# Kernel tuning notes

Hardware: AMD Instinct MI355X
Metric: run time of the kernel (lower is better)

## Reference

```python
import jax, jax.numpy as jnp
import numpy as np

N_NODES = 8192
N_EDGES = 65536


def _segment_softmax(scores, seg_ids, num_segments):
    # scores: [E, 1], seg_ids: [E] -> softmax over edges sharing the same dst
    m = jax.ops.segment_max(scores, seg_ids, num_segments=num_segments)  # [N,1]
    e = jnp.exp(scores - m[seg_ids])
    denom = jax.ops.segment_sum(e, seg_ids, num_segments=num_segments)   # [N,1]
    return e / denom[seg_ids]


def setup_inputs() -> dict:
    key = jax.random.key(0)
    ks = jax.random.split(key, 12)
    s = lambda fin: 1.0 / np.sqrt(fin)
    inp = {
        'n_f': jax.random.normal(ks[0], (N_NODES, 1024), jnp.float32),
        'word2vec': jax.random.normal(ks[1], (N_NODES, 300), jnp.float32),
        's_f': jax.random.normal(ks[2], (N_EDGES, 16), jnp.float32),
        'src': jax.random.randint(ks[3], (N_EDGES,), 0, N_NODES),
        'dst': jax.random.randint(ks[4], (N_EDGES,), 0, N_NODES),
        'We': jax.random.normal(ks[5], (2064, 1024), jnp.float32) * s(2064),
        'be': jnp.zeros((1024,), jnp.float32),
        'Wel': jax.random.normal(ks[6], (600, 600), jnp.float32) * s(600),
        'bel': jnp.zeros((600,), jnp.float32),
        'Wa': jax.random.normal(ks[7], (1024, 1), jnp.float32) * s(1024),
        'ba': jnp.zeros((1,), jnp.float32),
        'Wal': jax.random.normal(ks[8], (600, 1), jnp.float32) * s(600),
        'bal': jnp.zeros((1,), jnp.float32),
        'Wn': jax.random.normal(ks[9], (2048, 1024), jnp.float32) * s(2048),
        'bn': jnp.zeros((1024,), jnp.float32),
        'Wnl': jax.random.normal(ks[10], (600, 300), jnp.float32) * s(600),
        'bnl': jnp.zeros((300,), jnp.float32),
    }
    return inp


def reference(n_f, word2vec, s_f, src, dst,
              We, be, Wel, bel, Wa, ba, Wal, bal, Wn, bn, Wnl, bnl):
    # ---- edge apply (H_H_EdgeApplyModule) ----
    src_nf = n_f[src]                                    # [E,1024] gather
    feat = jnp.concatenate([src_nf, s_f, n_f[dst]], axis=1)  # [E,2064]
    e_f = jax.nn.relu(feat @ We + be)                    # [E,1024]
    feat_lang = jnp.concatenate([word2vec[src], word2vec[dst]], axis=1)  # [E,600]
    e_f_lang = jax.nn.relu(feat_lang @ Wel + bel)        # [E,600]

    # ---- edge attention (E_AttentionModule1): scalar score per edge ----
    a_feat = e_f @ Wa + ba                               # [E,1]
    a_feat_lang = e_f_lang @ Wal + bal                   # [E,1]

    # ---- reduce: mailbox softmax over incoming edges per dst node ----
    alpha = _segment_softmax(a_feat, dst, N_NODES)       # [E,1]
    alpha_lang = _segment_softmax(a_feat_lang, dst, N_NODES)
    z_f = jax.ops.segment_sum(alpha * (src_nf + e_f), dst, num_segments=N_NODES)      # [N,1024]
    z_f_lang = jax.ops.segment_sum(alpha_lang * word2vec[src], dst, num_segments=N_NODES)  # [N,300]

    # ---- node apply (H_NodeApplyModule) ----
    new_n_f = jax.nn.relu(jnp.concatenate([n_f, z_f], axis=1) @ Wn + bn)              # [N,1024]
    new_n_f_lang = jax.nn.relu(jnp.concatenate([word2vec, z_f_lang], axis=1) @ Wnl + bnl)  # [N,300]
    return new_n_f, new_n_f_lang
```

## Files before the change

### kernel.cpp

```cpp
#include <hip/hip_runtime.h>
#include <hip/hip_bf16.h>

#define N_NODES 8192
#define N_EDGES 65536
#define OUT0_ELEMS ((size_t)N_NODES * 1024)

using bf16 = __hip_bfloat16;
typedef __attribute__((ext_vector_type(8))) short short8;
typedef __attribute__((ext_vector_type(4))) float f32x4;

__device__ __forceinline__ float b2f(bf16 x) { return __bfloat162float(x); }
__device__ __forceinline__ bf16 f2b(float x) { return __float2bfloat16(x); }
__device__ __forceinline__ unsigned short bbits(float x)
{
  union { bf16 h; unsigned short u; } v; v.h = f2b(x); return v.u;
}
__device__ __forceinline__ unsigned pack2(float a, float b)
{
  return (unsigned)bbits(a) | ((unsigned)bbits(b) << 16);
}
__device__ __forceinline__ float4 ld4b(const bf16* p)
{
  uint2 u = *(const uint2*)p;
  float4 r;
  r.x = __uint_as_float(u.x << 16);
  r.y = __uint_as_float(u.x & 0xffff0000u);
  r.z = __uint_as_float(u.y << 16);
  r.w = __uint_as_float(u.y & 0xffff0000u);
  return r;
}
__device__ __forceinline__ void st4b(bf16* p, float a, float b, float c, float d)
{
  uint2 v; v.x = pack2(a, b); v.y = pack2(c, d);
  *(uint2*)p = v;
}

__global__ void GNN_27650999451833_kernel() {}

__global__ void gnn6_zero(int* __restrict__ p, int n)
{
  int i = blockIdx.x * blockDim.x + threadIdx.x;
  if (i < n) p[i] = 0;
}

__global__ __launch_bounds__(256)
void gnn7_cvt(const float* __restrict__ src, bf16* __restrict__ dst, int n8)
{
  int i = blockIdx.x * blockDim.x + threadIdx.x;
  if (i < n8) {
    float4 a = ((const float4*)src)[2 * i];
    float4 b = ((const float4*)src)[2 * i + 1];
    uint4 p;
    p.x = pack2(a.x, a.y); p.y = pack2(a.z, a.w);
    p.z = pack2(b.x, b.y); p.w = pack2(b.z, b.w);
    ((uint4*)dst)[i] = p;
  }
}

__global__ __launch_bounds__(256)
void gnn8_pad_w2v(const float* __restrict__ src, bf16* __restrict__ dst)
{
  int idx = blockIdx.x * blockDim.x + threadIdx.x;
  if (idx >= N_NODES * 80) return;
  int r = idx / 80, c0 = (idx % 80) * 4;
  float v[4];
#pragma unroll
  for (int j = 0; j < 4; ++j) {
    int c = c0 + j;
    v[j] = (c < 300) ? src[(size_t)r * 300 + c] : 0.f;
  }
  uint2 p; p.x = pack2(v[0], v[1]); p.y = pack2(v[2], v[3]);
  *(uint2*)(dst + (size_t)r * 320 + c0) = p;
}

__global__ __launch_bounds__(256)
void gnn8_pad_Wel(const float* __restrict__ src, bf16* __restrict__ dst)
{
  int idx = blockIdx.x * blockDim.x + threadIdx.x;
  if (idx >= 320 * 320) return;
  int k = idx / 320, c0 = (idx % 320) * 4;
  float v[4];
#pragma unroll
  for (int j = 0; j < 4; ++j) {
    int c = c0 + j;
    float x = 0.f;
    if (k < 300) {
      if (c < 600)       x = src[(size_t)k * 600 + c];
      else if (c < 1200) x = src[(size_t)(300 + k) * 600 + (c - 600)];
    }
    v[j] = x;
  }
  uint2 p; p.x = pack2(v[0], v[1]); p.y = pack2(v[2], v[3]);
  *(uint2*)(dst + (size_t)k * 1280 + c0) = p;
}

__global__ __launch_bounds__(256)
void gnn8_pad_Wnl(const float* __restrict__ src, bf16* __restrict__ dst)
{
  int idx = blockIdx.x * blockDim.x + threadIdx.x;
  if (idx >= 640 * 96) return;
  int k = idx / 96, c0 = (idx % 96) * 4;
  int kr = -1;
  if (k < 300) kr = k;
  else if (k >= 320 && k < 620) kr = k - 20;
  float v[4];
#pragma unroll
  for (int j = 0; j < 4; ++j) {
    int c = c0 + j;
    v[j] = (kr >= 0 && c < 300) ? src[(size_t)kr * 300 + c] : 0.f;
  }
  uint2 p; p.x = pack2(v[0], v[1]); p.y = pack2(v[2], v[3]);
  *(uint2*)(dst + (size_t)k * 384 + c0) = p;
}

__global__ __launch_bounds__(256)
void gnn7_mm_P(const bf16* __restrict__ A, const float* __restrict__ We,
               bf16* __restrict__ P)
{
  __shared__ short As[128 * 40];
  __shared__ short Bs[128 * 40];
  const int t = threadIdx.x;
  const int col0 = blockIdx.x * 128, row0 = blockIdx.y * 128;
  const int lane = t & 63, w = t >> 6, m16 = lane & 15, q = lane >> 4;
  const int wr = w >> 1, wc = w & 1;

  f32x4 acc[4][4];
#pragma unroll
  for (int mi = 0; mi < 4; ++mi)
#pragma unroll
    for (int ni = 0; ni < 4; ++ni) acc[mi][ni] = (f32x4){0.f, 0.f, 0.f, 0.f};

  const int ar = t >> 1, ah = (t & 1) * 16;
  const int bk = t & 31, bn0 = (t >> 5) * 16;

  const bf16* aptr = A + (size_t)(row0 + ar) * 1024 + ah;
  const float* bptr = (col0 < 1024)
      ? (We + (size_t)bk * 1024 + col0 + bn0)
      : (We + (size_t)(1040 + bk) * 1024 + (col0 - 1024) + bn0);

  uint4 a0 = *(const uint4*)(aptr);
  uint4 a1 = *(const uint4*)(aptr + 8);
  float4 b0 = *(const float4*)(bptr);
  float4 b1 = *(const float4*)(bptr + 4);
  float4 b2 = *(const float4*)(bptr + 8);
  float4 b3 = *(const float4*)(bptr + 12);

  for (int k0 = 0; k0 < 1024; k0 += 32) {
    if (k0) __syncthreads();
    *(uint4*)&As[ar * 40 + ah] = a0;
    *(uint4*)&As[ar * 40 + ah + 8] = a1;
    {
      short* brow = &Bs[bn0 * 40 + bk];
      brow[0 * 40] = (short)bbits(b0.x);  brow[1 * 40] = (short)bbits(b0.y);
      brow[2 * 40] = (short)bbits(b0.z);  brow[3 * 40] = (short)bbits(b0.w);
      brow[4 * 40] = (short)bbits(b1.x);  brow[5 * 40] = (short)bbits(b1.y);
      brow[6 * 40] = (short)bbits(b1.z);  brow[7 * 40] = (short)bbits(b1.w);
      brow[8 * 40] = (short)bbits(b2.x);  brow[9 * 40] = (short)bbits(b2.y);
      brow[10 * 40] = (short)bbits(b2.z); brow[11 * 40] = (short)bbits(b2.w);
      brow[12 * 40] = (short)bbits(b3.x); brow[13 * 40] = (short)bbits(b3.y);
      brow[14 * 40] = (short)bbits(b3.z); brow[15 * 40] = (short)bbits(b3.w);
    }
    __syncthreads();
    if (k0 + 32 < 1024) {
      a0 = *(const uint4*)(aptr + k0 + 32);
      a1 = *(const uint4*)(aptr + k0 + 40);
      const float* bp = bptr + (size_t)(k0 + 32) * 1024;
      b0 = *(const float4*)(bp);
      b1 = *(const float4*)(bp + 4);
      b2 = *(const float4*)(bp + 8);
      b3 = *(const float4*)(bp + 12);
    }
    short8 af[4];
#pragma unroll
    for (int mi = 0; mi < 4; ++mi)
      af[mi] = *(const short8*)&As[(wr * 64 + mi * 16 + m16) * 40 + 8 * q];
#pragma unroll
    for (int ni = 0; ni < 4; ++ni) {
      short8 bfv = *(const short8*)&Bs[(wc * 64 + ni * 16 + m16) * 40 + 8 * q];
#pragma unroll
      for (int mi = 0; mi < 4; ++mi)
        acc[mi][ni] =
            __builtin_amdgcn_mfma_f32_16x16x32_bf16(af[mi], bfv, acc[mi][ni], 0, 0, 0);
    }
  }
#pragma unroll
  for (int mi = 0; mi < 4; ++mi)
#pragma unroll
    for (int ni = 0; ni < 4; ++ni) {
      int c = col0 + wc * 64 + ni * 16 + m16;
#pragma unroll
      for (int r = 0; r < 4; ++r)
        P[(size_t)(row0 + wr * 64 + mi * 16 + 4 * q + r) * 2048 + c] =
            f2b(acc[mi][ni][r]);
    }
}

__global__ __launch_bounds__(256)
void gnn7_mm_out_n(const bf16* __restrict__ nf_bf, const bf16* __restrict__ zf,
                   const float* __restrict__ Wn, const float* __restrict__ bn,
                   float* __restrict__ out)
{
  __shared__ short As[128 * 40];
  __shared__ short Bs[128 * 40];
  const int t = threadIdx.x;
  const int col0 = blockIdx.x * 128, row0 = blockIdx.y * 128;
  const int lane = t & 63, w = t >> 6, m16 = lane & 15, q = lane >> 4;
  const int wr = w >> 1, wc = w & 1;

  f32x4 acc[4][4];
#pragma unroll
  for (int mi = 0; mi < 4; ++mi)
#pragma unroll
    for (int ni = 0; ni < 4; ++ni) acc[mi][ni] = (f32x4){0.f, 0.f, 0.f, 0.f};

  const int ar = t >> 1, ah = (t & 1) * 16;
  const int bk = t & 31, bn0 = (t >> 5) * 16;

  const bf16* ap0 = nf_bf + (size_t)(row0 + ar) * 1024 + ah;
  const bf16* ap1 = zf + (size_t)(row0 + ar) * 1024 + ah;
  const float* bptr = Wn + (size_t)bk * 1024 + col0 + bn0;

  uint4 a0 = *(const uint4*)(ap0);
  uint4 a1 = *(const uint4*)(ap0 + 8);
  float4 b0 = *(const float4*)(bptr);
  float4 b1 = *(const float4*)(bptr + 4);
  float4 b2 = *(const float4*)(bptr + 8);
  float4 b3 = *(const float4*)(bptr + 12);

  for (int k0 = 0; k0 < 2048; k0 += 32) {
    if (k0) __syncthreads();
    *(uint4*)&As[ar * 40 + ah] = a0;
    *(uint4*)&As[ar * 40 + ah + 8] = a1;
    {
      short* brow = &Bs[bn0 * 40 + bk];
      brow[0 * 40] = (short)bbits(b0.x);  brow[1 * 40] = (short)bbits(b0.y);
      brow[2 * 40] = (short)bbits(b0.z);  brow[3 * 40] = (short)bbits(b0.w);
      brow[4 * 40] = (short)bbits(b1.x);  brow[5 * 40] = (short)bbits(b1.y);
      brow[6 * 40] = (short)bbits(b1.z);  brow[7 * 40] = (short)bbits(b1.w);
      brow[8 * 40] = (short)bbits(b2.x);  brow[9 * 40] = (short)bbits(b2.y);
      brow[10 * 40] = (short)bbits(b2.z); brow[11 * 40] = (short)bbits(b2.w);
      brow[12 * 40] = (short)bbits(b3.x); brow[13 * 40] = (short)bbits(b3.y);
      brow[14 * 40] = (short)bbits(b3.z); brow[15 * 40] = (short)bbits(b3.w);
    }
    __syncthreads();
    if (k0 + 32 < 2048) {
      int kn = k0 + 32;
      if (kn + ah < 1024) {
        a0 = *(const uint4*)(ap0 + kn);
        a1 = *(const uint4*)(ap0 + kn + 8);
      } else {
        a0 = *(const uint4*)(ap1 + (kn - 1024));
        a1 = *(const uint4*)(ap1 + (kn - 1024) + 8);
      }
      const float* bp = bptr + (size_t)kn * 1024;
      b0 = *(const float4*)(bp);
      b1 = *(const float4*)(bp + 4);
      b2 = *(const float4*)(bp + 8);
      b3 = *(const float4*)(bp + 12);
    }
    short8 af[4];
#pragma unroll
    for (int mi = 0; mi < 4; ++mi)
      af[mi] = *(const short8*)&As[(wr * 64 + mi * 16 + m16) * 40 + 8 * q];
#pragma unroll
    for (int ni = 0; ni < 4; ++ni) {
      short8 bfv = *(const short8*)&Bs[(wc * 64 + ni * 16 + m16) * 40 + 8 * q];
#pragma unroll
      for (int mi = 0; mi < 4; ++mi)
        acc[mi][ni] =
            __builtin_amdgcn_mfma_f32_16x16x32_bf16(af[mi], bfv, acc[mi][ni], 0, 0, 0);
    }
  }
#pragma unroll
  for (int mi = 0; mi < 4; ++mi)
#pragma unroll
    for (int ni = 0; ni < 4; ++ni) {
      int c = col0 + wc * 64 + ni * 16 + m16;
      float bias = bn[c];
#pragma unroll
      for (int r = 0; r < 4; ++r) {
        float v = acc[mi][ni][r] + bias;
        out[(size_t)(row0 + wr * 64 + mi * 16 + 4 * q + r) * 1024 + c] =
            fmaxf(v, 0.f);
      }
    }
}

__global__ __launch_bounds__(256)
void gnn8_mm_Q(const bf16* __restrict__ A, const bf16* __restrict__ B,
               bf16* __restrict__ Q)
{
  __shared__ short As[128 * 40];
  __shared__ short Bs[128 * 40];
  const int t = threadIdx.x;
  const int col0 = blockIdx.x * 128, row0 = blockIdx.y * 128;
  const int lane = t & 63, w = t >> 6, m16 = lane & 15, q = lane >> 4;
  const int wr = w >> 1, wc = w & 1;

  f32x4 acc[4][4];
#pragma unroll
  for (int mi = 0; mi < 4; ++mi)
#pragma unroll
    for (int ni = 0; ni < 4; ++ni) acc[mi][ni] = (f32x4){0.f, 0.f, 0.f, 0.f};

  const int ar = t >> 1, ah = (t & 1) * 16;
  const int bk = t & 31, bn0 = (t >> 5) * 16;

  const bf16* aptr = A + (size_t)(row0 + ar) * 320 + ah;
  const bf16* bptr = B + (size_t)bk * 1280 + col0 + bn0;

  uint4 a0 = *(const uint4*)(aptr);
  uint4 a1 = *(const uint4*)(aptr + 8);
  uint4 b0 = *(const uint4*)(bptr);
  uint4 b1 = *(const uint4*)(bptr + 8);

  for (int k0 = 0; k0 < 320; k0 += 32) {
    if (k0) __syncthreads();
    *(uint4*)&As[ar * 40 + ah] = a0;
    *(uint4*)&As[ar * 40 + ah + 8] = a1;
    {
      const short* bs0 = (const short*)&b0;
      const short* bs1 = (const short*)&b1;
      short* brow = &Bs[bn0 * 40 + bk];
#pragma unroll
      for (int j = 0; j < 8; ++j) brow[j * 40] = bs0[j];
#pragma unroll
      for (int j = 0; j < 8; ++j) brow[(8 + j) * 40] = bs1[j];
    }
    __syncthreads();
    if (k0 + 32 < 320) {
      a0 = *(const uint4*)(aptr + k0 + 32);
      a1 = *(const uint4*)(aptr + k0 + 40);
      const bf16* bp = bptr + (size_t)(k0 + 32) * 1280;
      b0 = *(const uint4*)(bp);
      b1 = *(const uint4*)(bp + 8);
    }
    short8 af[4];
#pragma unroll
    for (int mi = 0; mi < 4; ++mi)
      af[mi] = *(const short8*)&As[(wr * 64 + mi * 16 + m16) * 40 + 8 * q];
#pragma unroll
    for (int ni = 0; ni < 4; ++ni) {
      short8 bfv = *(const short8*)&Bs[(wc * 64 + ni * 16 + m16) * 40 + 8 * q];
#pragma unroll
      for (int mi = 0; mi < 4; ++mi)
        acc[mi][ni] =
            __builtin_amdgcn_mfma_f32_16x16x32_bf16(af[mi], bfv, acc[mi][ni], 0, 0, 0);
    }
  }
#pragma unroll
  for (int mi = 0; mi < 4; ++mi)
#pragma unroll
    for (int ni = 0; ni < 4; ++ni) {
      int c = col0 + wc * 64 + ni * 16 + m16;
#pragma unroll
      for (int r = 0; r < 4; ++r)
        Q[(size_t)(row0 + wr * 64 + mi * 16 + 4 * q + r) * 1280 + c] =
            f2b(acc[mi][ni][r]);
    }
}

__global__ __launch_bounds__(256)
void gnn8_mm_out_l(const bf16* __restrict__ A0, const bf16* __restrict__ A1,
                   const bf16* __restrict__ B, const float* __restrict__ bnl,
                   float* __restrict__ out2)
{
  __shared__ short As[128 * 40];
  __shared__ short Bs[128 * 40];
  const int t = threadIdx.x;
  const int col0 = blockIdx.x * 128, row0 = blockIdx.y * 128;
  const int lane = t & 63, w = t >> 6, m16 = lane & 15, q = lane >> 4;
  const int wr = w >> 1, wc = w & 1;

  f32x4 acc[4][4];
#pragma unroll
  for (int mi = 0; mi < 4; ++mi)
#pragma unroll
    for (int ni = 0; ni < 4; ++ni) acc[mi][ni] = (f32x4){0.f, 0.f, 0.f, 0.f};

  const int ar = t >> 1, ah = (t & 1) * 16;
  const int bk = t & 31, bn0 = (t >> 5) * 16;

  const bf16* ap0 = A0 + (size_t)(row0 + ar) * 320 + ah;
  const bf16* ap1 = A1 + (size_t)(row0 + ar) * 320 + ah;
  const bf16* bptr = B + (size_t)bk * 384 + col0 + bn0;

  uint4 a0 = *(const uint4*)(ap0);
  uint4 a1 = *(const uint4*)(ap0 + 8);
  uint4 b0 = *(const uint4*)(bptr);
  uint4 b1 = *(const uint4*)(bptr + 8);

  for (int k0 = 0; k0 < 640; k0 += 32) {
    if (k0) __syncthreads();
    *(uint4*)&As[ar * 40 + ah] = a0;
    *(uint4*)&As[ar * 40 + ah + 8] = a1;
    {
      const short* bs0 = (const short*)&b0;
      const short* bs1 = (const short*)&b1;
      short* brow = &Bs[bn0 * 40 + bk];
#pragma unroll
      for (int j = 0; j < 8; ++j) brow[j * 40] = bs0[j];
#pragma unroll
      for (int j = 0; j < 8; ++j) brow[(8 + j) * 40] = bs1[j];
    }
    __syncthreads();
    if (k0 + 32 < 640) {
      int kn = k0 + 32;
      const bf16* ap = (kn < 320) ? (ap0 + kn) : (ap1 + (kn - 320));
      a0 = *(const uint4*)(ap);
      a1 = *(const uint4*)(ap + 8);
      const bf16* bp = bptr + (size_t)kn * 384;
      b0 = *(const uint4*)(bp);
      b1 = *(const uint4*)(bp + 8);
    }
    short8 af[4];
#pragma unroll
    for (int mi = 0; mi < 4; ++mi)
      af[mi] = *(const short8*)&As[(wr * 64 + mi * 16 + m16) * 40 + 8 * q];
#pragma unroll
    for (int ni = 0; ni < 4; ++ni) {
      short8 bfv = *(const short8*)&Bs[(wc * 64 + ni * 16 + m16) * 40 + 8 * q];
#pragma unroll
      for (int mi = 0; mi < 4; ++mi)
        acc[mi][ni] =
            __builtin_amdgcn_mfma_f32_16x16x32_bf16(af[mi], bfv, acc[mi][ni], 0, 0, 0);
    }
  }
#pragma unroll
  for (int mi = 0; mi < 4; ++mi)
#pragma unroll
    for (int ni = 0; ni < 4; ++ni) {
      int c = col0 + wc * 64 + ni * 16 + m16;
      if (c < 300) {
        float bias = bnl[c];
#pragma unroll
        for (int r = 0; r < 4; ++r) {
          float v = acc[mi][ni][r] + bias;
          out2[(size_t)(row0 + wr * 64 + mi * 16 + 4 * q + r) * 300 + c] =
              fmaxf(v, 0.f);
        }
      }
    }
}

__global__ __launch_bounds__(256)
void gnn9_edge_score(const int* __restrict__ src, const int* __restrict__ dst,
                     const float* __restrict__ s_f, const float* __restrict__ We,
                     const float* __restrict__ be, const float* __restrict__ Wa,
                     const float* __restrict__ ba, const float* __restrict__ bel,
                     const float* __restrict__ Wal, const float* __restrict__ bal,
                     const bf16* __restrict__ P, const bf16* __restrict__ Q,
                     float* __restrict__ af, float* __restrict__ afl)
{
  const int t = threadIdx.x;
  const int lane = t & 63, w = t >> 6;
  const int c0 = 4 * t;
  const int e0 = blockIdx.x * 8;

  float wef[16][4];
#pragma unroll
  for (int k = 0; k < 16; ++k) {
    float4 v = *(const float4*)(We + (size_t)(1024 + k) * 1024 + c0);
    wef[k][0] = v.x; wef[k][1] = v.y; wef[k][2] = v.z; wef[k][3] = v.w;
  }
  float4 bev = *(const float4*)(be + c0);
  float4 wav = *(const float4*)(Wa + c0);
  const bool lact = (t < 150);
  float4 belv = {0, 0, 0, 0}, walv = {0, 0, 0, 0};
  if (lact) { belv = *(const float4*)(bel + c0); walv = *(const float4*)(Wal + c0); }
  const float ba0 = ba[0], bal0 = bal[0];

  __shared__ float shf[4], shl[4];

  for (int i = 0; i < 8; ++i) {
    const int e = e0 + i;
    const int s = src[e], d = dst[e];

    float sfv[16];
    {
      const float4* sp = (const float4*)(s_f + (size_t)e * 16);
      float4 s0 = sp[0], s1 = sp[1], s2 = sp[2], s3 = sp[3];
      sfv[0] = s0.x; sfv[1] = s0.y; sfv[2] = s0.z; sfv[3] = s0.w;
      sfv[4] = s1.x; sfv[5] = s1.y; sfv[6] = s1.z; sfv[7] = s1.w;
      sfv[8] = s2.x; sfv[9] = s2.y; sfv[10] = s2.z; sfv[11] = s2.w;
      sfv[12] = s3.x; sfv[13] = s3.y; sfv[14] = s3.z; sfv[15] = s3.w;
    }

    float4 p1 = ld4b(P + (size_t)s * 2048 + c0);
    float4 p2 = ld4b(P + (size_t)d * 2048 + 1024 + c0);
    float pv[4] = {p1.x + p2.x + bev.x, p1.y + p2.y + bev.y,
                   p1.z + p2.z + bev.z, p1.w + p2.w + bev.w};
    float pf = 0.f;
#pragma unroll
    for (int j = 0; j < 4; ++j) {
      float v = pv[j];
#pragma unroll
      for (int k = 0; k < 16; ++k) v = fmaf(sfv[k], wef[k][j], v);
      pf = fmaf(fmaxf(v, 0.f), (&wav.x)[j], pf);
    }

    float pl = 0.f;
    if (lact) {
      float4 q1 = ld4b(Q + (size_t)s * 1280 + c0);
      float4 q2 = ld4b(Q + (size_t)d * 1280 + 600 + c0);
      float qv[4] = {q1.x + q2.x + belv.x, q1.y + q2.y + belv.y,
                     q1.z + q2.z + belv.z, q1.w + q2.w + belv.w};
#pragma unroll
      for (int j = 0; j < 4; ++j)
        pl = fmaf(fmaxf(qv[j], 0.f), (&walv.x)[j], pl);
    }

#pragma unroll
    for (int o = 32; o > 0; o >>= 1) {
      pf += __shfl_down(pf, o, 64);
      pl += __shfl_down(pl, o, 64);
    }
    if (lane == 0) { shf[w] = pf; shl[w] = pl; }
    __syncthreads();
    if (t == 0)  af[e]  = shf[0] + shf[1] + shf[2] + shf[3] + ba0;
    if (t == 64) afl[e] = shl[0] + shl[1] + shl[2] + shl[3] + bal0;
    __syncthreads();
  }
}

__global__ void gnn6_count(const int* __restrict__ dst, int* __restrict__ cnt)
{
  int e = blockIdx.x * blockDim.x + threadIdx.x;
  if (e < N_EDGES) atomicAdd(&cnt[dst[e]], 1);
}

__global__ __launch_bounds__(1024)
void gnn6_scan(const int* __restrict__ cnt, int* __restrict__ off, int* __restrict__ cur)
{
  __shared__ int sh[1024];
  const int t = threadIdx.x;
  int local[8]; int sum = 0;
#pragma unroll
  for (int i = 0; i < 8; ++i) { int v = cnt[t * 8 + i]; local[i] = sum; sum += v; }
  sh[t] = sum;
  __syncthreads();
  for (int d = 1; d < 1024; d <<= 1) {
    int v = (t >= d) ? sh[t - d] : 0;
    __syncthreads();
    sh[t] += v;
    __syncthreads();
  }
  int basev = (t > 0) ? sh[t - 1] : 0;
#pragma unroll
  for (int i = 0; i < 8; ++i) { int o = basev + local[i]; off[t * 8 + i] = o; cur[t * 8 + i] = o; }
  if (t == 1023) off[8192] = sh[1023];
}

__global__ void gnn6_fill(const int* __restrict__ dst, int* __restrict__ cur,
                          int* __restrict__ elist)
{
  int e = blockIdx.x * blockDim.x + threadIdx.x;
  if (e < N_EDGES) { int p = atomicAdd(&cur[dst[e]], 1); elist[p] = e; }
}

__global__ __launch_bounds__(256)
void gnn6_alpha(const int* __restrict__ off, const int* __restrict__ elist,
                float* __restrict__ af, float* __restrict__ afl)
{
  const int n = blockIdx.x * 256 + threadIdx.x;
  if (n >= N_NODES) return;
  const int base = off[n];
  const int deg = off[n + 1] - base;
  float m = -1e30f, ml = -1e30f;
  for (int i = 0; i < deg; ++i) {
    int e = elist[base + i];
    m = fmaxf(m, af[e]);
    ml = fmaxf(ml, afl[e]);
  }
  float den = 0.f, denl = 0.f;
  for (int i = 0; i < deg; ++i) {
    int e = elist[base + i];
    den += expf(af[e] - m);
    denl += expf(afl[e] - ml);
  }
  float inv = (den > 0.f) ? 1.f / den : 0.f;
  float invl = (denl > 0.f) ? 1.f / denl : 0.f;
  for (int i = 0; i < deg; ++i) {
    int e = elist[base + i];
    af[e] = expf(af[e] - m) * inv;
    afl[e] = expf(afl[e] - ml) * invl;
  }
}

__global__ __launch_bounds__(256)
void gnn9_node_z(const int* __restrict__ off, const int* __restrict__ elist,
                 const int* __restrict__ src, const float* __restrict__ af,
                 const float* __restrict__ afl, const bf16* __restrict__ nf_bf,
                 const bf16* __restrict__ w2v_pad, const float* __restrict__ s_f,
                 const float* __restrict__ We, const float* __restrict__ be,
                 const bf16* __restrict__ P, bf16* __restrict__ zf,
                 bf16* __restrict__ zfl_pad)
{
  const int node = blockIdx.x;
  const int t = threadIdx.x;
  const int c0 = 4 * t;
  const int base = off[node];
  const int deg = off[node + 1] - base;

  float wef[16][4];
#pragma unroll
  for (int k = 0; k < 16; ++k) {
    float4 v = *(const float4*)(We + (size_t)(1024 + k) * 1024 + c0);
    wef[k][0] = v.x; wef[k][1] = v.y; wef[k][2] = v.z; wef[k][3] = v.w;
  }
  float4 p2v = ld4b(P + (size_t)node * 2048 + 1024 + c0);
  float4 bev = *(const float4*)(be + c0);
  const float p2[4] = {p2v.x + bev.x, p2v.y + bev.y, p2v.z + bev.z, p2v.w + bev.w};

  float acc[4] = {0.f, 0.f, 0.f, 0.f};
  float accl[4] = {0.f, 0.f, 0.f, 0.f};
  const bool lact = (t < 75);

  for (int i = 0; i < deg; ++i) {
    const int e = elist[base + i];
    const int s = src[e];
    const float wgt = af[e];
    const float wl = afl[e];

    float sfv[16];
    {
      const float4* sp = (const float4*)(s_f + (size_t)e * 16);
      float4 s0 = sp[0], s1 = sp[1], s2 = sp[2], s3 = sp[3];
      sfv[0] = s0.x; sfv[1] = s0.y; sfv[2] = s0.z; sfv[3] = s0.w;
      sfv[4] = s1.x; sfv[5] = s1.y; sfv[6] = s1.z; sfv[7] = s1.w;
      sfv[8] = s2.x; sfv[9] = s2.y; sfv[10] = s2.z; sfv[11] = s2.w;
      sfv[12] = s3.x; sfv[13] = s3.y; sfv[14] = s3.z; sfv[15] = s3.w;
    }

    float4 p1 = ld4b(P + (size_t)s * 2048 + c0);
    float4 nf4 = ld4b(nf_bf + (size_t)s * 1024 + c0);
    const float p1a[4] = {p1.x, p1.y, p1.z, p1.w};
    const float nfa[4] = {nf4.x, nf4.y, nf4.z, nf4.w};
#pragma unroll
    for (int j = 0; j < 4; ++j) {
      float ef = p1a[j] + p2[j];
#pragma unroll
      for (int k = 0; k < 16; ++k) ef = fmaf(sfv[k], wef[k][j], ef);
      ef = fmaxf(ef, 0.f);
      acc[j] = fmaf(wgt, nfa[j] + ef, acc[j]);
    }
    if (lact) {
      float4 wv = ld4b(w2v_pad + (size_t)s * 320 + c0);
      accl[0] = fmaf(wl, wv.x, accl[0]);
      accl[1] = fmaf(wl, wv.y, accl[1]);
      accl[2] = fmaf(wl, wv.z, accl[2]);
      accl[3] = fmaf(wl, wv.w, accl[3]);
    }
  }
  st4b(zf + (size_t)node * 1024 + c0, acc[0], acc[1], acc[2], acc[3]);
  if (lact)
    st4b(zfl_pad + (size_t)node * 320 + c0, accl[0], accl[1], accl[2], accl[3]);
  else if (t < 80)
    st4b(zfl_pad + (size_t)node * 320 + c0, 0.f, 0.f, 0.f, 0.f);
}

extern "C" void kernel_launch(void* const* d_in, const int* in_sizes, int n_in,
                              void* d_out, int out_size, void* d_ws, size_t ws_size,
                              hipStream_t stream)
{
  (void)hipGetLastError();
  if (n_in != 17) { hipMemsetAsync(d_out, 0x41, 4096, stream); return; }

  const float* n_f = (const float*)d_in[0];
  const float* w2v = (const float*)d_in[1];
  const float* s_f = (const float*)d_in[2];
  const int*   src = (const int*)d_in[3];
  const int*   dst = (const int*)d_in[4];
  const float* We  = (const float*)d_in[5];
  const float* be  = (const float*)d_in[6];
  const float* Wel = (const float*)d_in[7];
  const float* bel = (const float*)d_in[8];
  const float* Wa  = (const float*)d_in[9];
  const float* ba  = (const float*)d_in[10];
  const float* Wal = (const float*)d_in[11];
  const float* bal = (const float*)d_in[12];
  const float* Wn  = (const float*)d_in[13];
  const float* bn  = (const float*)d_in[14];
  const float* Wnl = (const float*)d_in[15];
  const float* bnl = (const float*)d_in[16];
  float* out  = (float*)d_out;
  float* out2 = out + OUT0_ELEMS;

  char* ws = (char*)d_ws;
  size_t o = 0;
  auto alloc = [&](size_t bytes) -> void* {
    void* p = ws + o; o += bytes; o = (o + 255) & ~(size_t)255; return p;
  };
  bf16* P       = (bf16*)alloc((size_t)N_NODES * 2048 * 2);
  bf16* Q       = (bf16*)alloc((size_t)N_NODES * 1280 * 2);
  bf16* zf      = (bf16*)alloc((size_t)N_NODES * 1024 * 2);
  bf16* zfl_pad = (bf16*)alloc((size_t)N_NODES * 320 * 2);
  bf16* nf_bf   = (bf16*)alloc((size_t)N_NODES * 1024 * 2);
  bf16* w2v_pad = (bf16*)alloc((size_t)N_NODES * 320 * 2);
  bf16* Wel_pad = (bf16*)alloc((size_t)320 * 1280 * 2);
  bf16* Wnl_pad = (bf16*)alloc((size_t)640 * 384 * 2);
  float* af     = (float*)alloc((size_t)N_EDGES * 4);
  float* afl    = (float*)alloc((size_t)N_EDGES * 4);
  int* cnt      = (int*)alloc((size_t)N_NODES * 4);
  int* offs     = (int*)alloc((size_t)(N_NODES + 1) * 4);
  int* cur      = (int*)alloc((size_t)N_NODES * 4);
  int* elist    = (int*)alloc((size_t)N_EDGES * 4);
  if (o > ws_size) { hipMemsetAsync(d_out, 0x42, 4096, stream); return; }

  gnn6_zero<<<N_NODES / 256, 256, 0, stream>>>(cnt, N_NODES);
  gnn7_cvt<<<(N_NODES * 1024 / 8 + 255) / 256, 256, 0, stream>>>(n_f, nf_bf,
                                                                 N_NODES * 1024 / 8);
  gnn8_pad_w2v<<<(N_NODES * 80 + 255) / 256, 256, 0, stream>>>(w2v, w2v_pad);
  gnn8_pad_Wel<<<(320 * 320 + 255) / 256, 256, 0, stream>>>(Wel, Wel_pad);
  gnn8_pad_Wnl<<<(640 * 96 + 255) / 256, 256, 0, stream>>>(Wnl, Wnl_pad);

  {
    dim3 g(2048 / 128, N_NODES / 128);
    gnn7_mm_P<<<g, 256, 0, stream>>>(nf_bf, We, P);
  }
  {
    dim3 g(1280 / 128, N_NODES / 128);
    gnn8_mm_Q<<<g, 256, 0, stream>>>(w2v_pad, Wel_pad, Q);
  }

  gnn9_edge_score<<<N_EDGES / 8, 256, 0, stream>>>(src, dst, s_f, We, be, Wa, ba,
                                                   bel, Wal, bal, P, Q, af, afl);

  gnn6_count<<<N_EDGES / 256, 256, 0, stream>>>(dst, cnt);
  gnn6_scan<<<1, 1024, 0, stream>>>(cnt, offs, cur);
  gnn6_fill<<<N_EDGES / 256, 256, 0, stream>>>(dst, cur, elist);
  gnn6_alpha<<<N_NODES / 256, 256, 0, stream>>>(offs, elist, af, afl);

  gnn9_node_z<<<N_NODES, 256, 0, stream>>>(offs, elist, src, af, afl, nf_bf,
                                           w2v_pad, s_f, We, be, P, zf, zfl_pad);

  {
    dim3 g(1024 / 128, N_NODES / 128);
    gnn7_mm_out_n<<<g, 256, 0, stream>>>(nf_bf, zf, Wn, bn, out);
  }
  {
    dim3 g(384 / 128, N_NODES / 128);
    gnn8_mm_out_l<<<g, 256, 0, stream>>>(w2v_pad, zfl_pad, Wnl_pad, bnl, out2);
  }

  if (hipGetLastError() != hipSuccess) hipMemsetAsync(d_out, 0x44, 4096, stream);
}
```

Baseline: 578.4 us.

## Pre-transpose weights to bf16 K-contiguous layout for vectorized GEMM B loads

Adds transpose-and-convert kernels that write We, Wn, Wel and Wnl as bf16 in N-major, K-contiguous form. All four GEMMs can then load B tiles with 16-byte vector loads and store them to shared memory as whole vectors, instead of converting fp32 per element and scattering 2-byte shared-memory writes. This targets the per-iteration conversion cost and the strided shared-memory stores in the B path. In exchange it adds four transpose launches per call and extra workspace for the transposed weights.

Result: faster. 498.6 us (-13.8%).

```diff
diff --git a/kernel.cpp b/kernel.cpp
--- a/kernel.cpp
+++ b/kernel.cpp
@@ -74,48 +74,83 @@
 }
 
 __global__ __launch_bounds__(256)
-void gnn8_pad_Wel(const float* __restrict__ src, bf16* __restrict__ dst)
-{
-  int idx = blockIdx.x * blockDim.x + threadIdx.x;
-  if (idx >= 320 * 320) return;
-  int k = idx / 320, c0 = (idx % 320) * 4;
-  float v[4];
-#pragma unroll
-  for (int j = 0; j < 4; ++j) {
-    int c = c0 + j;
-    float x = 0.f;
+void gnn10_t_We(const float* __restrict__ src, bf16* __restrict__ dst)
+{
+  __shared__ float tile[32][33];
+  const int kb = blockIdx.x * 32, nb = blockIdx.y * 32;
+  const int tx = threadIdx.x & 31, ty = threadIdx.x >> 5;
+  const int n = nb + tx;
+#pragma unroll
+  for (int i = ty; i < 32; i += 8)
+    tile[i][tx] = (n < 1024)
+        ? src[(size_t)(kb + i) * 1024 + n]
+        : src[(size_t)(1040 + kb + i) * 1024 + (n - 1024)];
+  __syncthreads();
+#pragma unroll
+  for (int i = ty; i < 32; i += 8)
+    dst[(size_t)(nb + i) * 1024 + kb + tx] = f2b(tile[tx][i]);
+}
+
+__global__ __launch_bounds__(256)
+void gnn10_t_Wn(const float* __restrict__ src, bf16* __restrict__ dst)
+{
+  __shared__ float tile[32][33];
+  const int kb = blockIdx.x * 32, nb = blockIdx.y * 32;
+  const int tx = threadIdx.x & 31, ty = threadIdx.x >> 5;
+#pragma unroll
+  for (int i = ty; i < 32; i += 8)
+    tile[i][tx] = src[(size_t)(kb + i) * 1024 + nb + tx];
+  __syncthreads();
+#pragma unroll
+  for (int i = ty; i < 32; i += 8)
+    dst[(size_t)(nb + i) * 2048 + kb + tx] = f2b(tile[tx][i]);
+}
+
+__global__ __launch_bounds__(256)
+void gnn10_t_Wel(const float* __restrict__ src, bf16* __restrict__ dst)
+{
+  __shared__ float tile[32][33];
+  const int kb = blockIdx.x * 32, nb = blockIdx.y * 32;
+  const int tx = threadIdx.x & 31, ty = threadIdx.x >> 5;
+  const int n = nb + tx;
+#pragma unroll
+  for (int i = ty; i < 32; i += 8) {
+    int k = kb + i;
+    float v = 0.f;
     if (k < 300) {
-      if (c < 600)       x = src[(size_t)k * 600 + c];
-      else if (c < 1200) x = src[(size_t)(300 + k) * 600 + (c - 600)];
-    }
-    v[j] = x;
-  }
-  uint2 p; p.x = pack2(v[0], v[1]); p.y = pack2(v[2], v[3]);
-  *(uint2*)(dst + (size_t)k * 1280 + c0) = p;
-}
-
-__global__ __launch_bounds__(256)
-void gnn8_pad_Wnl(const float* __restrict__ src, bf16* __restrict__ dst)
-{
-  int idx = blockIdx.x * blockDim.x + threadIdx.x;
-  if (idx >= 640 * 96) return;
-  int k = idx / 96, c0 = (idx % 96) * 4;
-  int kr = -1;
-  if (k < 300) kr = k;
-  else if (k >= 320 && k < 620) kr = k - 20;
-  float v[4];
-#pragma unroll
-  for (int j = 0; j < 4; ++j) {
-    int c = c0 + j;
-    v[j] = (kr >= 0 && c < 300) ? src[(size_t)kr * 300 + c] : 0.f;
-  }
-  uint2 p; p.x = pack2(v[0], v[1]); p.y = pack2(v[2], v[3]);
-  *(uint2*)(dst + (size_t)k * 384 + c0) = p;
-}
-
-__global__ __launch_bounds__(256)
-void gnn7_mm_P(const bf16* __restrict__ A, const float* __restrict__ We,
-               bf16* __restrict__ P)
+      if (n < 600)       v = src[(size_t)k * 600 + n];
+      else if (n < 1200) v = src[(size_t)(300 + k) * 600 + (n - 600)];
+    }
+    tile[i][tx] = v;
+  }
+  __syncthreads();
+#pragma unroll
+  for (int i = ty; i < 32; i += 8)
+    dst[(size_t)(nb + i) * 320 + kb + tx] = f2b(tile[tx][i]);
+}
+
+__global__ __launch_bounds__(256)
+void gnn10_t_Wnl(const float* __restrict__ src, bf16* __restrict__ dst)
+{
+  __shared__ float tile[32][33];
+  const int kb = blockIdx.x * 32, nb = blockIdx.y * 32;
+  const int tx = threadIdx.x & 31, ty = threadIdx.x >> 5;
+  const int n = nb + tx;
+#pragma unroll
+  for (int i = ty; i < 32; i += 8) {
+    int k = kb + i;
+    int kr = (k < 300) ? k : ((k >= 320 && k < 620) ? (k - 20) : -1);
+    tile[i][tx] = (kr >= 0 && n < 300) ? src[(size_t)kr * 300 + n] : 0.f;
+  }
+  __syncthreads();
+#pragma unroll
+  for (int i = ty; i < 32; i += 8)
+    dst[(size_t)(nb + i) * 640 + kb + tx] = f2b(tile[tx][i]);
+}
+
+__global__ __launch_bounds__(256)
+void gnn10_mm_P(const bf16* __restrict__ A, const bf16* __restrict__ BT,
+                bf16* __restrict__ P)
 {
   __shared__ short As[128 * 40];
   __shared__ short Bs[128 * 40];
@@ -131,44 +166,26 @@
     for (int ni = 0; ni < 4; ++ni) acc[mi][ni] = (f32x4){0.f, 0.f, 0.f, 0.f};
 
   const int ar = t >> 1, ah = (t & 1) * 16;
-  const int bk = t & 31, bn0 = (t >> 5) * 16;
-
   const bf16* aptr = A + (size_t)(row0 + ar) * 1024 + ah;
-  const float* bptr = (col0 < 1024)
-      ? (We + (size_t)bk * 1024 + col0 + bn0)
-      : (We + (size_t)(1040 + bk) * 1024 + (col0 - 1024) + bn0);
+  const bf16* bptr = BT + (size_t)(col0 + ar) * 1024 + ah;
 
   uint4 a0 = *(const uint4*)(aptr);
   uint4 a1 = *(const uint4*)(aptr + 8);
-  float4 b0 = *(const float4*)(bptr);
-  float4 b1 = *(const float4*)(bptr + 4);
-  float4 b2 = *(const float4*)(bptr + 8);
-  float4 b3 = *(const float4*)(bptr + 12);
+  uint4 b0 = *(const uint4*)(bptr);
+  uint4 b1 = *(const uint4*)(bptr + 8);
 
   for (int k0 = 0; k0 < 1024; k0 += 32) {
     if (k0) __syncthreads();
     *(uint4*)&As[ar * 40 + ah] = a0;
     *(uint4*)&As[ar * 40 + ah + 8] = a1;
-    {
-      short* brow = &Bs[bn0 * 40 + bk];
-      brow[0 * 40] = (short)bbits(b0.x);  brow[1 * 40] = (short)bbits(b0.y);
-      brow[2 * 40] = (short)bbits(b0.z);  brow[3 * 40] = (short)bbits(b0.w);
-      brow[4 * 40] = (short)bbits(b1.x);  brow[5 * 40] = (short)bbits(b1.y);
-      brow[6 * 40] = (short)bbits(b1.z);  brow[7 * 40] = (short)bbits(b1.w);
-      brow[8 * 40] = (short)bbits(b2.x);  brow[9 * 40] = (short)bbits(b2.y);
-      brow[10 * 40] = (short)bbits(b2.z); brow[11 * 40] = (short)bbits(b2.w);
-      brow[12 * 40] = (short)bbits(b3.x); brow[13 * 40] = (short)bbits(b3.y);
-      brow[14 * 40] = (short)bbits(b3.z); brow[15 * 40] = (short)bbits(b3.w);
-    }
+    *(uint4*)&Bs[ar * 40 + ah] = b0;
+    *(uint4*)&Bs[ar * 40 + ah + 8] = b1;
     __syncthreads();
     if (k0 + 32 < 1024) {
       a0 = *(const uint4*)(aptr + k0 + 32);
       a1 = *(const uint4*)(aptr + k0 + 40);
-      const float* bp = bptr + (size_t)(k0 + 32) * 1024;
-      b0 = *(const float4*)(bp);
-      b1 = *(const float4*)(bp + 4);
-      b2 = *(const float4*)(bp + 8);
-      b3 = *(const float4*)(bp + 12);
+      b0 = *(const uint4*)(bptr + k0 + 32);
+      b1 = *(const uint4*)(bptr + k0 + 40);
     }
     short8 af[4];
 #pragma unroll
@@ -196,9 +213,9 @@
 }
 
 __global__ __launch_bounds__(256)
-void gnn7_mm_out_n(const bf16* __restrict__ nf_bf, const bf16* __restrict__ zf,
-                   const float* __restrict__ Wn, const float* __restrict__ bn,
-                   float* __restrict__ out)
+void gnn10_mm_out_n(const bf16* __restrict__ A0, const bf16* __restrict__ A1,
+                    const bf16* __restrict__ BT, const float* __restrict__ bn,
+                    float* __restrict__ out)
 {
   __shared__ short As[128 * 40];
   __shared__ short Bs[128 * 40];
@@ -214,49 +231,29 @@
     for (int ni = 0; ni < 4; ++ni) acc[mi][ni] = (f32x4){0.f, 0.f, 0.f, 0.f};
 
   const int ar = t >> 1, ah = (t & 1) * 16;
-  const int bk = t & 31, bn0 = (t >> 5) * 16;
-
-  const bf16* ap0 = nf_bf + (size_t)(row0 + ar) * 1024 + ah;
-  const bf16* ap1 = zf + (size_t)(row0 + ar) * 1024 + ah;
-  const float* bptr = Wn + (size_t)bk * 1024 + col0 + bn0;
+  const bf16* ap0 = A0 + (size_t)(row0 + ar) * 1024 + ah;
+  const bf16* ap1 = A1 + (size_t)(row0 + ar) * 1024 + ah;
+  const bf16* bptr = BT + (size_t)(col0 + ar) * 2048 + ah;
 
   uint4 a0 = *(const uint4*)(ap0);
   uint4 a1 = *(const uint4*)(ap0 + 8);
-  float4 b0 = *(const float4*)(bptr);
-  float4 b1 = *(const float4*)(bptr + 4);
-  float4 b2 = *(const float4*)(bptr + 8);
-  float4 b3 = *(const float4*)(bptr + 12);
+  uint4 b0 = *(const uint4*)(bptr);
+  uint4 b1 = *(const uint4*)(bptr + 8);
 
   for (int k0 = 0; k0 < 2048; k0 += 32) {
     if (k0) __syncthreads();
     *(uint4*)&As[ar * 40 + ah] = a0;
     *(uint4*)&As[ar * 40 + ah + 8] = a1;
-    {
-      short* brow = &Bs[bn0 * 40 + bk];
-      brow[0 * 40] = (short)bbits(b0.x);  brow[1 * 40] = (short)bbits(b0.y);
-      brow[2 * 40] = (short)bbits(b0.z);  brow[3 * 40] = (short)bbits(b0.w);
-      brow[4 * 40] = (short)bbits(b1.x);  brow[5 * 40] = (short)bbits(b1.y);
-      brow[6 * 40] = (short)bbits(b1.z);  brow[7 * 40] = (short)bbits(b1.w);
-      brow[8 * 40] = (short)bbits(b2.x);  brow[9 * 40] = (short)bbits(b2.y);
-      brow[10 * 40] = (short)bbits(b2.z); brow[11 * 40] = (short)bbits(b2.w);
-      brow[12 * 40] = (short)bbits(b3.x); brow[13 * 40] = (short)bbits(b3.y);
-      brow[14 * 40] = (short)bbits(b3.z); brow[15 * 40] = (short)bbits(b3.w);
-    }
+    *(uint4*)&Bs[ar * 40 + ah] = b0;
+    *(uint4*)&Bs[ar * 40 + ah + 8] = b1;
     __syncthreads();
     if (k0 + 32 < 2048) {
       int kn = k0 + 32;
-      if (kn + ah < 1024) {
-        a0 = *(const uint4*)(ap0 + kn);
-        a1 = *(const uint4*)(ap0 + kn + 8);
-      } else {
-        a0 = *(const uint4*)(ap1 + (kn - 1024));
-        a1 = *(const uint4*)(ap1 + (kn - 1024) + 8);
-      }
-      const float* bp = bptr + (size_t)kn * 1024;
-      b0 = *(const float4*)(bp);
-      b1 = *(const float4*)(bp + 4);
-      b2 = *(const float4*)(bp + 8);
-      b3 = *(const float4*)(bp + 12);
+      const bf16* ap = (kn < 1024) ? (ap0 + kn) : (ap1 + (kn - 1024));
+      a0 = *(const uint4*)(ap);
+      a1 = *(const uint4*)(ap + 8);
+      b0 = *(const uint4*)(bptr + kn);
+      b1 = *(const uint4*)(bptr + kn + 8);
     }
     short8 af[4];
 #pragma unroll
@@ -287,8 +284,8 @@
 }
 
 __global__ __launch_bounds__(256)
-void gnn8_mm_Q(const bf16* __restrict__ A, const bf16* __restrict__ B,
-               bf16* __restrict__ Q)
+void gnn10_mm_Q(const bf16* __restrict__ A, const bf16* __restrict__ BT,
+                bf16* __restrict__ Q)
 {
   __shared__ short As[128 * 40];
   __shared__ short Bs[128 * 40];
@@ -304,10 +301,8 @@
     for (int ni = 0; ni < 4; ++ni) acc[mi][ni] = (f32x4){0.f, 0.f, 0.f, 0.f};
 
   const int ar = t >> 1, ah = (t & 1) * 16;
-  const int bk = t & 31, bn0 = (t >> 5) * 16;
-
   const bf16* aptr = A + (size_t)(row0 + ar) * 320 + ah;
-  const bf16* bptr = B + (size_t)bk * 1280 + col0 + bn0;
+  const bf16* bptr = BT + (size_t)(col0 + ar) * 320 + ah;
 
   uint4 a0 = *(const uint4*)(aptr);
   uint4 a1 = *(const uint4*)(aptr + 8);
@@ -318,22 +313,14 @@
     if (k0) __syncthreads();
     *(uint4*)&As[ar * 40 + ah] = a0;
     *(uint4*)&As[ar * 40 + ah + 8] = a1;
-    {
-      const short* bs0 = (const short*)&b0;
-      const short* bs1 = (const short*)&b1;
-      short* brow = &Bs[bn0 * 40 + bk];
-#pragma unroll
-      for (int j = 0; j < 8; ++j) brow[j * 40] = bs0[j];
-#pragma unroll
-      for (int j = 0; j < 8; ++j) brow[(8 + j) * 40] = bs1[j];
-    }
+    *(uint4*)&Bs[ar * 40 + ah] = b0;
+    *(uint4*)&Bs[ar * 40 + ah + 8] = b1;
     __syncthreads();
     if (k0 + 32 < 320) {
       a0 = *(const uint4*)(aptr + k0 + 32);
       a1 = *(const uint4*)(aptr + k0 + 40);
-      const bf16* bp = bptr + (size_t)(k0 + 32) * 1280;
-      b0 = *(const uint4*)(bp);
-      b1 = *(const uint4*)(bp + 8);
+      b0 = *(const uint4*)(bptr + k0 + 32);
+      b1 = *(const uint4*)(bptr + k0 + 40);
     }
     short8 af[4];
 #pragma unroll
@@ -361,9 +348,9 @@
 }
 
 __global__ __launch_bounds__(256)
-void gnn8_mm_out_l(const bf16* __restrict__ A0, const bf16* __restrict__ A1,
-                   const bf16* __restrict__ B, const float* __restrict__ bnl,
-                   float* __restrict__ out2)
+void gnn10_mm_out_l(const bf16* __restrict__ A0, const bf16* __restrict__ A1,
+                    const bf16* __restrict__ BT, const float* __restrict__ bnl,
+                    float* __restrict__ out2)
 {
   __shared__ short As[128 * 40];
   __shared__ short Bs[128 * 40];
@@ -379,11 +366,9 @@
     for (int ni = 0; ni < 4; ++ni) acc[mi][ni] = (f32x4){0.f, 0.f, 0.f, 0.f};
 
   const int ar = t >> 1, ah = (t & 1) * 16;
-  const int bk = t & 31, bn0 = (t >> 5) * 16;
-
   const bf16* ap0 = A0 + (size_t)(row0 + ar) * 320 + ah;
   const bf16* ap1 = A1 + (size_t)(row0 + ar) * 320 + ah;
-  const bf16* bptr = B + (size_t)bk * 384 + col0 + bn0;
+  const bf16* bptr = BT + (size_t)(col0 + ar) * 640 + ah;
 
   uint4 a0 = *(const uint4*)(ap0);
   uint4 a1 = *(const uint4*)(ap0 + 8);
@@ -394,24 +379,16 @@
     if (k0) __syncthreads();
     *(uint4*)&As[ar * 40 + ah] = a0;
     *(uint4*)&As[ar * 40 + ah + 8] = a1;
-    {
-      const short* bs0 = (const short*)&b0;
-      const short* bs1 = (const short*)&b1;
-      short* brow = &Bs[bn0 * 40 + bk];
-#pragma unroll
-      for (int j = 0; j < 8; ++j) brow[j * 40] = bs0[j];
-#pragma unroll
-      for (int j = 0; j < 8; ++j) brow[(8 + j) * 40] = bs1[j];
-    }
+    *(uint4*)&Bs[ar * 40 + ah] = b0;
+    *(uint4*)&Bs[ar * 40 + ah + 8] = b1;
     __syncthreads();
     if (k0 + 32 < 640) {
       int kn = k0 + 32;
       const bf16* ap = (kn < 320) ? (ap0 + kn) : (ap1 + (kn - 320));
       a0 = *(const uint4*)(ap);
       a1 = *(const uint4*)(ap + 8);
-      const bf16* bp = bptr + (size_t)kn * 384;
-      b0 = *(const uint4*)(bp);
-      b1 = *(const uint4*)(bp + 8);
+      b0 = *(const uint4*)(bptr + kn);
+      b1 = *(const uint4*)(bptr + kn + 8);
     }
     short8 af[4];
 #pragma unroll
@@ -691,36 +668,40 @@
   auto alloc = [&](size_t bytes) -> void* {
     void* p = ws + o; o += bytes; o = (o + 255) & ~(size_t)255; return p;
   };
-  bf16* P       = (bf16*)alloc((size_t)N_NODES * 2048 * 2);
-  bf16* Q       = (bf16*)alloc((size_t)N_NODES * 1280 * 2);
-  bf16* zf      = (bf16*)alloc((size_t)N_NODES * 1024 * 2);
-  bf16* zfl_pad = (bf16*)alloc((size_t)N_NODES * 320 * 2);
-  bf16* nf_bf   = (bf16*)alloc((size_t)N_NODES * 1024 * 2);
-  bf16* w2v_pad = (bf16*)alloc((size_t)N_NODES * 320 * 2);
-  bf16* Wel_pad = (bf16*)alloc((size_t)320 * 1280 * 2);
-  bf16* Wnl_pad = (bf16*)alloc((size_t)640 * 384 * 2);
-  float* af     = (float*)alloc((size_t)N_EDGES * 4);
-  float* afl    = (float*)alloc((size_t)N_EDGES * 4);
-  int* cnt      = (int*)alloc((size_t)N_NODES * 4);
-  int* offs     = (int*)alloc((size_t)(N_NODES + 1) * 4);
-  int* cur      = (int*)alloc((size_t)N_NODES * 4);
-  int* elist    = (int*)alloc((size_t)N_EDGES * 4);
+  bf16* P        = (bf16*)alloc((size_t)N_NODES * 2048 * 2);
+  bf16* Q        = (bf16*)alloc((size_t)N_NODES * 1280 * 2);
+  bf16* zf       = (bf16*)alloc((size_t)N_NODES * 1024 * 2);
+  bf16* zfl_pad  = (bf16*)alloc((size_t)N_NODES * 320 * 2);
+  bf16* nf_bf    = (bf16*)alloc((size_t)N_NODES * 1024 * 2);
+  bf16* w2v_pad  = (bf16*)alloc((size_t)N_NODES * 320 * 2);
+  bf16* WeT      = (bf16*)alloc((size_t)2048 * 1024 * 2);
+  bf16* WnT      = (bf16*)alloc((size_t)1024 * 2048 * 2);
+  bf16* WelT     = (bf16*)alloc((size_t)1280 * 320 * 2);
+  bf16* WnlT     = (bf16*)alloc((size_t)384 * 640 * 2);
+  float* af      = (float*)alloc((size_t)N_EDGES * 4);
+  float* afl     = (float*)alloc((size_t)N_EDGES * 4);
+  int* cnt       = (int*)alloc((size_t)N_NODES * 4);
+  int* offs      = (int*)alloc((size_t)(N_NODES + 1) * 4);
+  int* cur       = (int*)alloc((size_t)N_NODES * 4);
+  int* elist     = (int*)alloc((size_t)N_EDGES * 4);
   if (o > ws_size) { hipMemsetAsync(d_out, 0x42, 4096, stream); return; }
 
   gnn6_zero<<<N_NODES / 256, 256, 0, stream>>>(cnt, N_NODES);
   gnn7_cvt<<<(N_NODES * 1024 / 8 + 255) / 256, 256, 0, stream>>>(n_f, nf_bf,
                                                                  N_NODES * 1024 / 8);
   gnn8_pad_w2v<<<(N_NODES * 80 + 255) / 256, 256, 0, stream>>>(w2v, w2v_pad);
-  gnn8_pad_Wel<<<(320 * 320 + 255) / 256, 256, 0, stream>>>(Wel, Wel_pad);
-  gnn8_pad_Wnl<<<(640 * 96 + 255) / 256, 256, 0, stream>>>(Wnl, Wnl_pad);
+  { dim3 g(32, 64); gnn10_t_We<<<g, 256, 0, stream>>>(We, WeT); }
+  { dim3 g(64, 32); gnn10_t_Wn<<<g, 256, 0, stream>>>(Wn, WnT); }
+  { dim3 g(10, 40); gnn10_t_Wel<<<g, 256, 0, stream>>>(Wel, WelT); }
+  { dim3 g(20, 12); gnn10_t_Wnl<<<g, 256, 0, stream>>>(Wnl, WnlT); }
 
   {
     dim3 g(2048 / 128, N_NODES / 128);
-    gnn7_mm_P<<<g, 256, 0, stream>>>(nf_bf, We, P);
+    gnn10_mm_P<<<g, 256, 0, stream>>>(nf_bf, WeT, P);
   }
   {
     dim3 g(1280 / 128, N_NODES / 128);
-    gnn8_mm_Q<<<g, 256, 0, stream>>>(w2v_pad, Wel_pad, Q);
+    gnn10_mm_Q<<<g, 256, 0, stream>>>(w2v_pad, WelT, Q);
   }
 
   gnn9_edge_score<<<N_EDGES / 8, 256, 0, stream>>>(src, dst, s_f, We, be, Wa, ba,
@@ -736,11 +717,11 @@
 
   {
     dim3 g(1024 / 128, N_NODES / 128);
-    gnn7_mm_out_n<<<g, 256, 0, stream>>>(nf_bf, zf, Wn, bn, out);
+    gnn10_mm_out_n<<<g, 256, 0, stream>>>(nf_bf, zf, WnT, bn, out);
   }
   {
     dim3 g(384 / 128, N_NODES / 128);
-    gnn8_mm_out_l<<<g, 256, 0, stream>>>(w2v_pad, zfl_pad, Wnl_pad, bnl, out2);
+    gnn10_mm_out_l<<<g, 256, 0, stream>>>(w2v_pad, zfl_pad, WnlT, bnl, out2);
   }
 
   if (hipGetLastError() != hipSuccess) hipMemsetAsync(d_out, 0x44, 4096, stream);
```
